# Kernel optimization log

Hardware: AMD Instinct MI355X
Metric: run time of the kernel (lower is better)

## Reference

```python
import jax, jax.numpy as jnp
import numpy as np

B, C, K = 128, 32, 128


def setup_inputs() -> dict:
    key = jax.random.key(0)
    k1, k2, k3, k4, k5 = jax.random.split(key, 5)
    x = jax.random.normal(k1, (B, 1, K, K), dtype=jnp.float32)
    # Conv2d(1, C, (1, K)) weight -> effectively [C, K] over the column axis
    w_col = jax.random.normal(k2, (C, K), dtype=jnp.float32) * (1.0 / np.sqrt(K))
    b_col = jax.random.normal(k3, (C,), dtype=jnp.float32) * 0.01
    # Conv2d(1, C, (K, 1)) weight -> effectively [C, K] over the row axis
    w_row = jax.random.normal(k4, (C, K), dtype=jnp.float32) * (1.0 / np.sqrt(K))
    b_row = jax.random.normal(k5, (C,), dtype=jnp.float32) * 0.01
    return {"x": x, "w_col": w_col, "b_col": b_col, "w_row": w_row, "b_row": b_row}


def reference(x, w_col, b_col, w_row, b_row):
    xs = x[:, 0]  # [B, K, K]
    # conv_column: kernel (1, K) contracts the column axis j -> [B, C, K] (rows i)
    col = jnp.einsum("bij,cj->bci", xs, w_col) + b_col[None, :, None]
    # conv_row: kernel (K, 1) contracts the row axis i -> [B, C, K] (cols j)
    row = jnp.einsum("bij,ci->bcj", xs, w_row) + b_row[None, :, None]
    # Tiling conv_row to [B,C,K,K] (identical rows) and conv_column to
    # [B,C,K,K] (identical columns) and matmul-ing yields, for every (i, j):
    #   out[b,c,i,j] = sum_k row[b,c,k] * col[b,c,k]
    # i.e. a per-(b,c) scalar broadcast over the K x K plane.
    s = jnp.einsum("bck,bck->bc", row, col)  # [B, C]
    return jnp.broadcast_to(s[:, :, None, None], (x.shape[0], w_col.shape[0], K, K))
```

## Files before the change

kernel.cpp:

```cpp
#include <hip/hip_runtime.h>
#include <hip/hip_bf16.h>


constexpr int KDIM = 128;
constexpr int CDIM = 32;
constexpr int XS_LD = 132;

__device__ __forceinline__ int swz_word(int row, int col) {
    return (row << 7) | ((((col >> 2) ^ ((row >> 2) & 7)) << 2) | (col & 3));
}

__global__ __launch_bounds__(256) void compute_s_kernel(
    const float* __restrict__ x,
    const float* __restrict__ w_col, const float* __restrict__ b_col,
    const float* __restrict__ w_row, const float* __restrict__ b_row,
    float* __restrict__ s_out)
{
    __shared__ float  xs[KDIM * XS_LD];
    __shared__ float  xt[KDIM * KDIM];
    __shared__ float2 wpr[KDIM][8];
    __shared__ float2 wpc[KDIM][8];

    const int b   = blockIdx.x >> 1;
    const int ch  = blockIdx.x & 1;
    const int tid = threadIdx.x;
    const int C0  = ch * 16;

    #pragma unroll
    for (int e = 0; e < 4; ++e) {
        const int idx = tid + 256 * e;
        const int i   = idx & 127;
        const int cg  = idx >> 7;
        wpr[i][cg] = make_float2(w_row[(C0 + cg) * KDIM + i],
                                 w_row[(C0 + cg + 8) * KDIM + i]);
        wpc[i][cg] = make_float2(w_col[(C0 + cg) * KDIM + i],
                                 w_col[(C0 + cg + 8) * KDIM + i]);
    }

    const float4* xsrc = reinterpret_cast<const float4*>(x + (size_t)b * KDIM * KDIM);
    const int tj  = tid & 31;
    const int ti0 = tid >> 5;
    #pragma unroll
    for (int it = 0; it < 4; ++it) {
        const int ti = ti0 + 8 * it;
        const float4 r0 = xsrc[(4 * ti + 0) * 32 + tj];
        const float4 r1 = xsrc[(4 * ti + 1) * 32 + tj];
        const float4 r2 = xsrc[(4 * ti + 2) * 32 + tj];
        const float4 r3 = xsrc[(4 * ti + 3) * 32 + tj];
        *reinterpret_cast<float4*>(&xs[(4 * ti + 0) * XS_LD + 4 * tj]) = r0;
        *reinterpret_cast<float4*>(&xs[(4 * ti + 1) * XS_LD + 4 * tj]) = r1;
        *reinterpret_cast<float4*>(&xs[(4 * ti + 2) * XS_LD + 4 * tj]) = r2;
        *reinterpret_cast<float4*>(&xs[(4 * ti + 3) * XS_LD + 4 * tj]) = r3;
        *reinterpret_cast<float4*>(&xt[swz_word(4 * tj + 0, 4 * ti)]) =
            make_float4(r0.x, r1.x, r2.x, r3.x);
        *reinterpret_cast<float4*>(&xt[swz_word(4 * tj + 1, 4 * ti)]) =
            make_float4(r0.y, r1.y, r2.y, r3.y);
        *reinterpret_cast<float4*>(&xt[swz_word(4 * tj + 2, 4 * ti)]) =
            make_float4(r0.z, r1.z, r2.z, r3.z);
        *reinterpret_cast<float4*>(&xt[swz_word(4 * tj + 3, 4 * ti)]) =
            make_float4(r0.w, r1.w, r2.w, r3.w);
    }
    __syncthreads();

    const int kq = tid & 31;
    const int cg = tid >> 5;

    float au0[4] = {0,0,0,0}, au1[4] = {0,0,0,0};
    float av0[4] = {0,0,0,0}, av1[4] = {0,0,0,0};

    #pragma unroll 4
    for (int i = 0; i < KDIM; ++i) {
        const float4 xv = *reinterpret_cast<const float4*>(&xs[i * XS_LD + 4 * kq]);
        const float4 tv = *reinterpret_cast<const float4*>(&xt[swz_word(i, 4 * kq)]);
        const float2 wu = wpr[i][cg];
        const float2 wv = wpc[i][cg];
        au0[0] = fmaf(wu.x, xv.x, au0[0]); au0[1] = fmaf(wu.x, xv.y, au0[1]);
        au0[2] = fmaf(wu.x, xv.z, au0[2]); au0[3] = fmaf(wu.x, xv.w, au0[3]);
        au1[0] = fmaf(wu.y, xv.x, au1[0]); au1[1] = fmaf(wu.y, xv.y, au1[1]);
        au1[2] = fmaf(wu.y, xv.z, au1[2]); au1[3] = fmaf(wu.y, xv.w, au1[3]);
        av0[0] = fmaf(wv.x, tv.x, av0[0]); av0[1] = fmaf(wv.x, tv.y, av0[1]);
        av0[2] = fmaf(wv.x, tv.z, av0[2]); av0[3] = fmaf(wv.x, tv.w, av0[3]);
        av1[0] = fmaf(wv.y, tv.x, av1[0]); av1[1] = fmaf(wv.y, tv.y, av1[1]);
        av1[2] = fmaf(wv.y, tv.z, av1[2]); av1[3] = fmaf(wv.y, tv.w, av1[3]);
    }

    const int c0 = C0 + cg, c1 = C0 + cg + 8;
    const float br0 = b_row[c0], bc0 = b_col[c0];
    const float br1 = b_row[c1], bc1 = b_col[c1];

    float p0 = 0.f, p1 = 0.f;
    #pragma unroll
    for (int q = 0; q < 4; ++q) {
        p0 += (au0[q] + br0) * (av0[q] + bc0);
        p1 += (au1[q] + br1) * (av1[q] + bc1);
    }
    #pragma unroll
    for (int off = 16; off; off >>= 1) {
        p0 += __shfl_xor(p0, off, 32);
        p1 += __shfl_xor(p1, off, 32);
    }
    if (kq == 0) {
        s_out[b * CDIM + c0] = p0;
        s_out[b * CDIM + c1] = p1;
    }
}

__global__ __launch_bounds__(256) void bcast_kernel(
    const float* __restrict__ s, float* __restrict__ out)
{
    #pragma unroll
    for (int slab = 0; slab < 2; ++slab) {
        const int bc = blockIdx.x * 2 + slab;
        const float val = s[bc];
        float4 v4;
        v4.x = v4.y = v4.z = v4.w = val;
        float4* o = reinterpret_cast<float4*>(out) + (size_t)bc * 4096;
        #pragma unroll
        for (int r = 0; r < 16; ++r) {
            o[threadIdx.x + 256 * r] = v4;
        }
    }
}

extern "C" void kernel_launch(void* const* d_in, const int* in_sizes, int n_in,
                              void* d_out, int out_size, void* d_ws, size_t ws_size,
                              hipStream_t stream) {
    const float* x     = (const float*)d_in[0];
    const float* w_col = (const float*)d_in[1];
    const float* b_col = (const float*)d_in[2];
    const float* w_row = (const float*)d_in[3];
    const float* b_row = (const float*)d_in[4];
    float* out  = (float*)d_out;
    float* s_ws = (float*)d_ws;

    compute_s_kernel<<<256, 256, 0, stream>>>(x, w_col, b_col, w_row, b_row, s_ws);
    bcast_kernel<<<2048, 256, 0, stream>>>(s_ws, out);
}
```

Baseline: 54.68 us.

## Fuse score computation and broadcast into one 512-thread kernel with XCD-aware mapping

Merges the compute and broadcast kernels into a single launch. Each block now computes its 16 channel scores, stages them in LDS and writes the broadcast planes itself, which removes the second launch and the workspace round trip. Blocks grow to 512 threads, with the row reduction split across the two half-waves and combined by a shuffle. Block indices are remapped so that consecutive batches land on the same XCD. The risk is that only 256 blocks now issue the 64 MB of output stores, where the old broadcast kernel spread them over 2048 blocks, so store throughput may drop.

```diff
diff --git a/kernel.cpp b/kernel.cpp
--- a/kernel.cpp
+++ b/kernel.cpp
@@ -4,53 +4,57 @@
 
 constexpr int KDIM = 128;
 constexpr int CDIM = 32;
-constexpr int XS_LD = 132;
+constexpr int LD   = 132;
 
 __device__ __forceinline__ int swz_word(int row, int col) {
     return (row << 7) | ((((col >> 2) ^ ((row >> 2) & 7)) << 2) | (col & 3));
 }
 
-__global__ __launch_bounds__(256) void compute_s_kernel(
+__global__ __launch_bounds__(512) void fused_kernel(
     const float* __restrict__ x,
     const float* __restrict__ w_col, const float* __restrict__ b_col,
     const float* __restrict__ w_row, const float* __restrict__ b_row,
-    float* __restrict__ s_out)
+    float* __restrict__ out)
 {
-    __shared__ float  xs[KDIM * XS_LD];
+    __shared__ float  xs[KDIM * LD];
     __shared__ float  xt[KDIM * KDIM];
     __shared__ float2 wpr[KDIM][8];
     __shared__ float2 wpc[KDIM][8];
+    __shared__ float  s_lds[16];
 
-    const int b   = blockIdx.x >> 1;
-    const int ch  = blockIdx.x & 1;
+    const int bid = blockIdx.x;
+    const int xcd = bid & 7;
+    const int idx = bid >> 3;
+    const int b   = xcd * 16 + (idx >> 1);
+    const int ch  = idx & 1;
+    const int C0  = ch * 16;
     const int tid = threadIdx.x;
-    const int C0  = ch * 16;
 
     #pragma unroll
-    for (int e = 0; e < 4; ++e) {
-        const int idx = tid + 256 * e;
-        const int i   = idx & 127;
-        const int cg  = idx >> 7;
-        wpr[i][cg] = make_float2(w_row[(C0 + cg) * KDIM + i],
-                                 w_row[(C0 + cg + 8) * KDIM + i]);
-        wpc[i][cg] = make_float2(w_col[(C0 + cg) * KDIM + i],
-                                 w_col[(C0 + cg + 8) * KDIM + i]);
+    for (int e = 0; e < 2; ++e) {
+        const int ent = tid + 512 * e;
+        const int i   = ent & 127;
+        const int g   = ent >> 7;
+        wpr[i][g] = make_float2(w_row[(C0 + g) * KDIM + i],
+                                w_row[(C0 + g + 8) * KDIM + i]);
+        wpc[i][g] = make_float2(w_col[(C0 + g) * KDIM + i],
+                                w_col[(C0 + g + 8) * KDIM + i]);
     }
 
     const float4* xsrc = reinterpret_cast<const float4*>(x + (size_t)b * KDIM * KDIM);
     const int tj  = tid & 31;
     const int ti0 = tid >> 5;
     #pragma unroll
-    for (int it = 0; it < 4; ++it) {
-        const int ti = ti0 + 8 * it;
+    for (int it = 0; it < 2; ++it) {
+        const int ti = ti0 + 16 * it;
         const float4 r0 = xsrc[(4 * ti + 0) * 32 + tj];
         const float4 r1 = xsrc[(4 * ti + 1) * 32 + tj];
         const float4 r2 = xsrc[(4 * ti + 2) * 32 + tj];
         const float4 r3 = xsrc[(4 * ti + 3) * 32 + tj];
-        *reinterpret_cast<float4*>(&xs[(4 * ti + 0) * XS_LD + 4 * tj]) = r0;
-        *reinterpret_cast<float4*>(&xs[(4 * ti + 1) * XS_LD + 4 * tj]) = r1;
-        *reinterpret_cast<float4*>(&xs[(4 * ti + 2) * XS_LD + 4 * tj]) = r2;
-        *reinterpret_cast<float4*>(&xs[(4 * ti + 3) * XS_LD + 4 * tj]) = r3;
+        *reinterpret_cast<float4*>(&xs[(4 * ti + 0) * LD + 4 * tj]) = r0;
+        *reinterpret_cast<float4*>(&xs[(4 * ti + 1) * LD + 4 * tj]) = r1;
+        *reinterpret_cast<float4*>(&xs[(4 * ti + 2) * LD + 4 * tj]) = r2;
+        *reinterpret_cast<float4*>(&xs[(4 * ti + 3) * LD + 4 * tj]) = r3;
         *reinterpret_cast<float4*>(&xt[swz_word(4 * tj + 0, 4 * ti)]) =
             make_float4(r0.x, r1.x, r2.x, r3.x);
         *reinterpret_cast<float4*>(&xt[swz_word(4 * tj + 1, 4 * ti)]) =
@@ -62,18 +66,22 @@
     }
     __syncthreads();
 
-    const int kq = tid & 31;
-    const int cg = tid >> 5;
+    const int w    = tid >> 6;
+    const int lane = tid & 63;
+    const int kq   = lane & 31;
+    const int ih   = lane >> 5;
+    const int k0   = 4 * kq;
 
     float au0[4] = {0,0,0,0}, au1[4] = {0,0,0,0};
     float av0[4] = {0,0,0,0}, av1[4] = {0,0,0,0};
 
     #pragma unroll 4
-    for (int i = 0; i < KDIM; ++i) {
-        const float4 xv = *reinterpret_cast<const float4*>(&xs[i * XS_LD + 4 * kq]);
-        const float4 tv = *reinterpret_cast<const float4*>(&xt[swz_word(i, 4 * kq)]);
-        const float2 wu = wpr[i][cg];
-        const float2 wv = wpc[i][cg];
+    for (int ii = 0; ii < 64; ++ii) {
+        const int i = ih * 64 + ii;
+        const float4 xv = *reinterpret_cast<const float4*>(&xs[i * LD + k0]);
+        const float4 tv = *reinterpret_cast<const float4*>(&xt[swz_word(i, k0)]);
+        const float2 wu = wpr[i][w];
+        const float2 wv = wpc[i][w];
         au0[0] = fmaf(wu.x, xv.x, au0[0]); au0[1] = fmaf(wu.x, xv.y, au0[1]);
         au0[2] = fmaf(wu.x, xv.z, au0[2]); au0[3] = fmaf(wu.x, xv.w, au0[3]);
         au1[0] = fmaf(wu.y, xv.x, au1[0]); au1[1] = fmaf(wu.y, xv.y, au1[1]);
@@ -84,7 +92,14 @@
         av1[2] = fmaf(wv.y, tv.z, av1[2]); av1[3] = fmaf(wv.y, tv.w, av1[3]);
     }
 
-    const int c0 = C0 + cg, c1 = C0 + cg + 8;
+    #pragma unroll
+    for (int q = 0; q < 4; ++q) {
+        au0[q] += __shfl_xor(au0[q], 32);
+        au1[q] += __shfl_xor(au1[q], 32);
+        av0[q] += __shfl_xor(av0[q], 32);
+        av1[q] += __shfl_xor(av1[q], 32);
+    }
+    const int c0 = C0 + w, c1 = C0 + w + 8;
     const float br0 = b_row[c0], bc0 = b_col[c0];
     const float br1 = b_row[c1], bc1 = b_col[c1];
 
@@ -95,29 +110,23 @@
         p1 += (au1[q] + br1) * (av1[q] + bc1);
     }
     #pragma unroll
-    for (int off = 16; off; off >>= 1) {
-        p0 += __shfl_xor(p0, off, 32);
-        p1 += __shfl_xor(p1, off, 32);
+    for (int off = 1; off < 32; off <<= 1) {
+        p0 += __shfl_xor(p0, off);
+        p1 += __shfl_xor(p1, off);
     }
-    if (kq == 0) {
-        s_out[b * CDIM + c0] = p0;
-        s_out[b * CDIM + c1] = p1;
-    }
-}
+    if (lane == 0) { s_lds[w] = p0; s_lds[w + 8] = p1; }
+    __syncthreads();
 
-__global__ __launch_bounds__(256) void bcast_kernel(
-    const float* __restrict__ s, float* __restrict__ out)
-{
+    float4* out4 = reinterpret_cast<float4*>(out);
     #pragma unroll
-    for (int slab = 0; slab < 2; ++slab) {
-        const int bc = blockIdx.x * 2 + slab;
-        const float val = s[bc];
+    for (int cl = 0; cl < 16; ++cl) {
+        const float val = s_lds[cl];
         float4 v4;
         v4.x = v4.y = v4.z = v4.w = val;
-        float4* o = reinterpret_cast<float4*>(out) + (size_t)bc * 4096;
+        float4* o = out4 + (size_t)(b * CDIM + C0 + cl) * 4096;
         #pragma unroll
-        for (int r = 0; r < 16; ++r) {
-            o[threadIdx.x + 256 * r] = v4;
+        for (int r = 0; r < 8; ++r) {
+            o[tid + 512 * r] = v4;
         }
     }
 }
@@ -130,9 +139,7 @@
     const float* b_col = (const float*)d_in[2];
     const float* w_row = (const float*)d_in[3];
     const float* b_row = (const float*)d_in[4];
-    float* out  = (float*)d_out;
-    float* s_ws = (float*)d_ws;
+    float* out = (float*)d_out;
 
-    compute_s_kernel<<<256, 256, 0, stream>>>(x, w_col, b_col, w_row, b_row, s_ws);
-    bcast_kernel<<<2048, 256, 0, stream>>>(s_ws, out);
+    fused_kernel<<<256, 512, 0, stream>>>(x, w_col, b_col, w_row, b_row, out);
 }
```

Result: faster. 52.20 us (-4.5%).
